# Kernel tuning notes

Hardware: AMD Instinct MI355X
Metric: run time of the kernel (lower is better)

The kernel has to match this reference:

```python
import jax, jax.numpy as jnp
import numpy as np

N, E = 50000, 250000
HID, H, C, IN, ED, L = 64, 4, 64, 6, 4, 2  # C = per-head out_channels


def _layer_norm(x, g, b, eps=1e-5):
    m = x.mean(-1, keepdims=True)
    v = x.var(-1, keepdims=True)
    return (x - m) / jnp.sqrt(v + eps) * g + b


def setup_inputs() -> dict:
    key = jax.random.key(0)
    ks = iter(jax.random.split(key, 32))
    rn = lambda shape, s=0.05: (jax.random.normal(next(ks), shape, dtype=jnp.float32) * s)
    inp = {
        "x": rn((N, IN), 1.0),
        "edge_index": jax.random.randint(next(ks), (2, E), 0, N, dtype=jnp.int64),
        "edge_attr": rn((E, ED), 1.0),
        "enc_w1": rn((IN, HID)), "enc_b1": jnp.zeros((HID,), jnp.float32),
        "enc_ln_g": jnp.ones((HID,), jnp.float32), "enc_ln_b": jnp.zeros((HID,), jnp.float32),
        "enc_w2": rn((HID, HID)), "enc_b2": jnp.zeros((HID,), jnp.float32),
        "Wq": rn((L, HID, H * C)), "bq": jnp.zeros((L, H * C), jnp.float32),
        "Wk": rn((L, HID, H * C)), "bk": jnp.zeros((L, H * C), jnp.float32),
        "Wv": rn((L, HID, H * C)), "bv": jnp.zeros((L, H * C), jnp.float32),
        "We": rn((L, ED, H * C)),
        "Wskip": rn((L, HID, HID)), "bskip": jnp.zeros((L, HID), jnp.float32),
        "Wbeta": rn((L, 3 * HID, 1)),
        "ln_g": jnp.ones((L, HID), jnp.float32), "ln_b": jnp.zeros((L, HID), jnp.float32),
        "head_w1": rn((HID, HID // 2)), "head_b1": jnp.zeros((HID // 2,), jnp.float32),
        "head_w2": rn((HID // 2, 2)), "head_b2": jnp.zeros((2,), jnp.float32),
    }
    return inp


def _transformer_conv(h, src, dst, ea, Wq, bq, Wk, bk, Wv, bv, We, Ws, bs, Wb):
    n = h.shape[0]
    q = (h @ Wq + bq).reshape(n, H, C)
    k = (h @ Wk + bk).reshape(n, H, C)
    v = (h @ Wv + bv).reshape(n, H, C)
    e = (ea @ We).reshape(-1, H, C)          # [E,H,C] edge projection (no bias)
    kj = k[src] + e                           # gather keys at source + edge
    alpha = (q[dst] * kj).sum(-1) / jnp.sqrt(jnp.float32(C))   # [E,H]
    # segment softmax over edges sharing a destination node
    m = jax.ops.segment_max(alpha, dst, num_segments=n)
    m = jnp.where(jnp.isfinite(m), m, 0.0)
    ex = jnp.exp(alpha - m[dst])
    s = jax.ops.segment_sum(ex, dst, num_segments=n)
    attn = ex / (s[dst] + 1e-16)              # [E,H]
    msg = (v[src] + e) * attn[:, :, None]
    out = jax.ops.segment_sum(msg, dst, num_segments=n).mean(axis=1)  # concat=False -> head mean
    xr = h @ Ws + bs                          # skip projection
    beta = jax.nn.sigmoid(jnp.concatenate([out, xr, out - xr], axis=-1) @ Wb)  # [N,1]
    return beta * xr + (1.0 - beta) * out


def reference(x, edge_index, edge_attr, enc_w1, enc_b1, enc_ln_g, enc_ln_b, enc_w2, enc_b2,
              Wq, bq, Wk, bk, Wv, bv, We, Wskip, bskip, Wbeta, ln_g, ln_b,
              head_w1, head_b1, head_w2, head_b2):
    src, dst = edge_index[0], edge_index[1]
    # node encoder (dropout = identity in eval)
    h = jax.nn.gelu(x @ enc_w1 + enc_b1, approximate=False)
    h = _layer_norm(h, enc_ln_g, enc_ln_b)
    h = h @ enc_w2 + enc_b2
    # stacked TransformerConv + residual + LayerNorm
    for l in range(Wq.shape[0]):
        h_new = _transformer_conv(h, src, dst, edge_attr,
                                  Wq[l], bq[l], Wk[l], bk[l], Wv[l], bv[l],
                                  We[l], Wskip[l], bskip[l], Wbeta[l])
        h = _layer_norm(h + h_new, ln_g[l], ln_b[l])
    # output head
    o = jax.nn.gelu(h @ head_w1 + head_b1, approximate=False)
    return o @ head_w2 + head_b2
```

## Files before the change

kernel.cpp:

```cpp
#include <hip/hip_runtime.h>
#include <hip/hip_bf16.h>
#include <math.h>

#define NN 50000
#define EE 250000
#define SBLK 256
#define NBLK ((NN + SBLK - 1) / SBLK)

typedef __attribute__((ext_vector_type(8))) short bf16x8;
typedef __attribute__((ext_vector_type(4))) float f32x4;

__device__ __forceinline__ float wsum64(float v) {
  v += __shfl_xor(v, 1, 64);
  v += __shfl_xor(v, 2, 64);
  v += __shfl_xor(v, 4, 64);
  v += __shfl_xor(v, 8, 64);
  v += __shfl_xor(v, 16, 64);
  v += __shfl_xor(v, 32, 64);
  return v;
}

__device__ __forceinline__ int wsum64i(int v) {
  v += __shfl_xor(v, 1, 64);
  v += __shfl_xor(v, 2, 64);
  v += __shfl_xor(v, 4, 64);
  v += __shfl_xor(v, 8, 64);
  v += __shfl_xor(v, 16, 64);
  v += __shfl_xor(v, 32, 64);
  return v;
}

__device__ __forceinline__ int wscan_inc(int v, int lane) {
  #pragma unroll
  for (int d = 1; d < 64; d <<= 1) {
    int u = __shfl_up(v, d, 64);
    if (lane >= d) v += u;
  }
  return v;
}

__device__ __forceinline__ float gelu_exact(float a) {
  return 0.5f * a * (1.0f + erff(a * 0.70710678118654752f));
}

__device__ __forceinline__ ushort f2bf(float f) {
  __hip_bfloat16 h = __float2bfloat16(f);
  return *reinterpret_cast<ushort*>(&h);
}

__device__ __forceinline__ void bf4_to_f(const uint2 u, float* f) {
  f[0] = __uint_as_float(u.x << 16);
  f[1] = __uint_as_float(u.x & 0xffff0000u);
  f[2] = __uint_as_float(u.y << 16);
  f[3] = __uint_as_float(u.y & 0xffff0000u);
}

__global__ __launch_bounds__(256) void convert_wb_kernel(
    const float* __restrict__ Wq, const float* __restrict__ Wk,
    const float* __restrict__ Wv, const float* __restrict__ Ws,
    __hip_bfloat16* __restrict__ Wb) {
  const int tid = blockIdx.x * 256 + threadIdx.x;
  const int layer = tid / 53248;
  const int rem = tid % 53248;
  const int i = rem & 7;
  const int l = (rem >> 3) & 63;
  const int fct = rem >> 9;
  const int f = fct & 1;
  const int ct = fct >> 1;
  const int col = ct * 16 + (l & 15);
  const int kk = f * 32 + (l >> 4) * 8 + i;
  float val;
  if (col < 256)      val = Wq[(size_t)layer * 16384 + kk * 256 + col];
  else if (col < 512) val = Wk[(size_t)layer * 16384 + kk * 256 + (col - 256)];
  else if (col < 768) val = Wv[(size_t)layer * 16384 + kk * 256 + (col - 512)];
  else                val = Ws[(size_t)layer * 4096 + kk * 64 + (col - 768)];
  Wb[tid] = __float2bfloat16(val);
}

__global__ __launch_bounds__(256) void hist_kernel(const int* __restrict__ ei,
                                                   int* __restrict__ cnt) {
  const int e = blockIdx.x * 256 + threadIdx.x;
  if (e < EE) atomicAdd(&cnt[ei[EE + e]], 1);
}

__global__ __launch_bounds__(256) void bsum_kernel(const int* __restrict__ cnt,
                                                   int* __restrict__ bsum) {
  const int i = blockIdx.x * 256 + threadIdx.x;
  int v = (i < NN) ? cnt[i] : 0;
  v = wsum64i(v);
  __shared__ int ws_[4];
  if ((threadIdx.x & 63) == 0) ws_[threadIdx.x >> 6] = v;
  __syncthreads();
  if (threadIdx.x == 0) bsum[blockIdx.x] = ws_[0] + ws_[1] + ws_[2] + ws_[3];
}

__global__ __launch_bounds__(256) void bscan_kernel(const int* __restrict__ bsum,
                                                    int* __restrict__ bpre) {
  const int t = threadIdx.x;
  const int lane = t & 63;
  const int w = t >> 6;
  int orig = (t < NBLK) ? bsum[t] : 0;
  int v = wscan_inc(orig, lane);
  __shared__ int wtot[4];
  if (lane == 63) wtot[w] = v;
  __syncthreads();
  int add = 0;
  #pragma unroll
  for (int j = 0; j < 4; j++) if (j < w) add += wtot[j];
  if (t < NBLK) bpre[t] = v + add - orig;
}

__global__ __launch_bounds__(256) void scan2_kernel(const int* __restrict__ cnt,
                                                    const int* __restrict__ bpre,
                                                    int* __restrict__ offs,
                                                    int* __restrict__ cursor) {
  const int i = blockIdx.x * 256 + threadIdx.x;
  const int t = threadIdx.x;
  const int lane = t & 63;
  const int w = t >> 6;
  int orig = (i < NN) ? cnt[i] : 0;
  int v = wscan_inc(orig, lane);
  __shared__ int wtot[4];
  if (lane == 63) wtot[w] = v;
  __syncthreads();
  int add = bpre[blockIdx.x];
  #pragma unroll
  for (int j = 0; j < 4; j++) if (j < w) add += wtot[j];
  int ex = v + add - orig;
  if (i < NN) { offs[i] = ex; cursor[i] = ex; }
  if (i == 0) offs[NN] = EE;
}

__global__ __launch_bounds__(256) void scatter_kernel(
    const int* __restrict__ ei, const float* __restrict__ ea,
    int* __restrict__ cursor, int* __restrict__ src_sorted,
    float4* __restrict__ ea_sorted) {
  const int e = blockIdx.x * 256 + threadIdx.x;
  if (e >= EE) return;
  const int dst = ei[EE + e];
  const int pos = atomicAdd(&cursor[dst], 1);
  src_sorted[pos] = ei[e];
  ea_sorted[pos] = reinterpret_cast<const float4*>(ea)[e];
}

__global__ __launch_bounds__(256) void enc_kernel(
    const float* __restrict__ x, const float* __restrict__ w1,
    const float* __restrict__ b1, const float* __restrict__ lg,
    const float* __restrict__ lb, const float* __restrict__ w2,
    const float* __restrict__ b2, float* __restrict__ h,
    __hip_bfloat16* __restrict__ hb) {
  const int t = blockIdx.x * 256 + threadIdx.x;
  const int node = t >> 6;
  const int lane = t & 63;
  const int wib = (threadIdx.x >> 6);
  __shared__ float gS[4][64];
  if (node < NN) {
    float a = b1[lane];
    #pragma unroll
    for (int d = 0; d < 6; d++) a += x[(size_t)node * 6 + d] * w1[d * 64 + lane];
    float g = gelu_exact(a);
    float s1 = wsum64(g);
    float s2 = wsum64(g * g);
    float m = s1 * (1.0f / 64.0f);
    float var = s2 * (1.0f / 64.0f) - m * m;
    g = (g - m) * rsqrtf(var + 1e-5f) * lg[lane] + lb[lane];
    gS[wib][lane] = g;
  }
  __syncthreads();
  if (node < NN) {
    float a = b2[lane];
    #pragma unroll 8
    for (int d = 0; d < 64; d++) a += gS[wib][d] * w2[d * 64 + lane];
    h[(size_t)node * 64 + lane] = a;
    hb[(size_t)node * 64 + lane] = __float2bfloat16(a);
  }
}

__global__ __launch_bounds__(256) void proj_mfma_kernel(
    const __hip_bfloat16* __restrict__ hbf,
    const __hip_bfloat16* __restrict__ Wb,
    const float* __restrict__ bq, const float* __restrict__ bk,
    const float* __restrict__ bv, const float* __restrict__ bs,
    __hip_bfloat16* __restrict__ q, __hip_bfloat16* __restrict__ k,
    __hip_bfloat16* __restrict__ v, float* __restrict__ xr) {
  const int n0 = blockIdx.x * 64;
  const int w = threadIdx.x >> 6;
  const int l = threadIdx.x & 63;
  const int r = l & 15;
  const int g = l >> 4;
  const int node = n0 + w * 16 + r;
  const int cg = g * 4;
  const bool in = (node < NN);

  bf16x8 A0 = {}, A1 = {};
  if (in) {
    const bf16x8* ap = reinterpret_cast<const bf16x8*>(hbf + (size_t)node * 64);
    A0 = ap[g];
    A1 = ap[g + 4];
  }

  const bf16x8* wb = reinterpret_cast<const bf16x8*>(Wb);

  for (int ct = 0; ct < 52; ++ct) {
    bf16x8 B0 = wb[(ct * 2 + 0) * 64 + l];
    bf16x8 B1 = wb[(ct * 2 + 1) * 64 + l];
    f32x4 acc = {0.f, 0.f, 0.f, 0.f};
    acc = __builtin_amdgcn_mfma_f32_16x16x32_bf16(B0, A0, acc, 0, 0, 0);
    acc = __builtin_amdgcn_mfma_f32_16x16x32_bf16(B1, A1, acc, 0, 0, 0);
    if (!in) continue;
    if (ct < 48) {
      __hip_bfloat16* dstp;
      const float* bias;
      int cb;
      float scale = 1.0f;
      if (ct < 16)      { dstp = q; bias = bq; cb = ct * 16 + cg; scale = 0.125f; }
      else if (ct < 32) { dstp = k; bias = bk; cb = (ct - 16) * 16 + cg; }
      else              { dstp = v; bias = bv; cb = (ct - 32) * 16 + cg; }
      const float4 bb = *reinterpret_cast<const float4*>(bias + cb);
      uint2 pk;
      pk.x = (uint)f2bf((acc[0] + bb.x) * scale) |
             ((uint)f2bf((acc[1] + bb.y) * scale) << 16);
      pk.y = (uint)f2bf((acc[2] + bb.z) * scale) |
             ((uint)f2bf((acc[3] + bb.w) * scale) << 16);
      *reinterpret_cast<uint2*>(dstp + (size_t)node * 256 + cb) = pk;
    } else {
      const int cb = (ct - 48) * 16 + cg;
      const float4 bb = *reinterpret_cast<const float4*>(bs + cb);
      float4 o = {acc[0] + bb.x, acc[1] + bb.y, acc[2] + bb.z, acc[3] + bb.w};
      *reinterpret_cast<float4*>(xr + (size_t)node * 64 + cb) = o;
    }
  }
}

__global__ __launch_bounds__(256) void edge_fused_kernel(
    const int* __restrict__ offs, const int* __restrict__ src_sorted,
    const float4* __restrict__ ea_sorted,
    const __hip_bfloat16* __restrict__ qb, const __hip_bfloat16* __restrict__ kb,
    const __hip_bfloat16* __restrict__ vb, const float* __restrict__ We,
    float* __restrict__ agg) {
  const int node = (blockIdx.x * 256 + threadIdx.x) >> 6;
  const int lane = threadIdx.x & 63;
  if (node >= NN) return;
  const int c0 = lane * 4;
  const ushort* q = reinterpret_cast<const ushort*>(qb);
  const ushort* k = reinterpret_cast<const ushort*>(kb);
  const ushort* v = reinterpret_cast<const ushort*>(vb);

  const float4 w0 = *reinterpret_cast<const float4*>(We + 0 * 256 + c0);
  const float4 w1 = *reinterpret_cast<const float4*>(We + 1 * 256 + c0);
  const float4 w2 = *reinterpret_cast<const float4*>(We + 2 * 256 + c0);
  const float4 w3 = *reinterpret_cast<const float4*>(We + 3 * 256 + c0);

  const int beg = offs[node];
  const int end = offs[node + 1];
  float qf[4];
  {
    uint2 qu = *reinterpret_cast<const uint2*>(q + (size_t)node * 256 + c0);
    bf4_to_f(qu, qf);
  }
  float m0 = 0.f, m1 = 0.f, m2 = 0.f, m3 = 0.f, sacc = 0.f;
  for (int e = beg; e < end; ++e) {
    const int src = src_sorted[e];
    const float4 av = ea_sorted[e];
    const float eh0 = av.x * w0.x + av.y * w1.x + av.z * w2.x + av.w * w3.x;
    const float eh1 = av.x * w0.y + av.y * w1.y + av.z * w2.y + av.w * w3.y;
    const float eh2 = av.x * w0.z + av.y * w1.z + av.z * w2.z + av.w * w3.z;
    const float eh3 = av.x * w0.w + av.y * w1.w + av.z * w2.w + av.w * w3.w;
    uint2 ku = *reinterpret_cast<const uint2*>(k + (size_t)src * 256 + c0);
    uint2 vu = *reinterpret_cast<const uint2*>(v + (size_t)src * 256 + c0);
    float kf[4], vf[4];
    bf4_to_f(ku, kf);
    bf4_to_f(vu, vf);
    float d = qf[0] * (kf[0] + eh0) + qf[1] * (kf[1] + eh1) +
              qf[2] * (kf[2] + eh2) + qf[3] * (kf[3] + eh3);
    d += __shfl_xor(d, 1, 64);
    d += __shfl_xor(d, 2, 64);
    d += __shfl_xor(d, 4, 64);
    d += __shfl_xor(d, 8, 64);
    const float ex = __expf(d);
    sacc += ex;
    m0 += ex * (vf[0] + eh0);
    m1 += ex * (vf[1] + eh1);
    m2 += ex * (vf[2] + eh2);
    m3 += ex * (vf[3] + eh3);
  }
  const float inv = 0.25f / (sacc + 1e-16f);
  m0 *= inv; m1 *= inv; m2 *= inv; m3 *= inv;
  m0 += __shfl_xor(m0, 16, 64); m0 += __shfl_xor(m0, 32, 64);
  m1 += __shfl_xor(m1, 16, 64); m1 += __shfl_xor(m1, 32, 64);
  m2 += __shfl_xor(m2, 16, 64); m2 += __shfl_xor(m2, 32, 64);
  m3 += __shfl_xor(m3, 16, 64); m3 += __shfl_xor(m3, 32, 64);
  if (lane < 16) {
    float4 o = {m0, m1, m2, m3};
    *reinterpret_cast<float4*>(agg + (size_t)node * 64 + lane * 4) = o;
  }
}

__global__ __launch_bounds__(256) void node_kernel(
    const float* __restrict__ agg, const float* __restrict__ xr,
    float* __restrict__ h, __hip_bfloat16* __restrict__ hb,
    const float* __restrict__ Wb,
    const float* __restrict__ lg, const float* __restrict__ lb) {
  const int t = blockIdx.x * 256 + threadIdx.x;
  const int node = t >> 6;
  const int lane = t & 63;
  if (node >= NN) return;
  float o = agg[(size_t)node * 64 + lane];
  float x = xr[(size_t)node * 64 + lane];
  float p = o * Wb[lane] + x * Wb[64 + lane] + (o - x) * Wb[128 + lane];
  p = wsum64(p);
  float beta = 1.0f / (1.0f + expf(-p));
  float hn = beta * x + (1.0f - beta) * o;
  float val = h[(size_t)node * 64 + lane] + hn;
  float s1 = wsum64(val);
  float s2 = wsum64(val * val);
  float m = s1 * (1.0f / 64.0f);
  float var = s2 * (1.0f / 64.0f) - m * m;
  float res = (val - m) * rsqrtf(var + 1e-5f) * lg[lane] + lb[lane];
  h[(size_t)node * 64 + lane] = res;
  hb[(size_t)node * 64 + lane] = __float2bfloat16(res);
}

__global__ __launch_bounds__(256) void head_kernel(
    const float* __restrict__ h, const float* __restrict__ w1,
    const float* __restrict__ b1, const float* __restrict__ w2,
    const float* __restrict__ b2, float* __restrict__ out) {
  const int base_node = blockIdx.x * 8;
  const int nib = threadIdx.x >> 5;
  const int c = threadIdx.x & 31;
  __shared__ float hS[8][64];
  #pragma unroll
  for (int i = 0; i < 2; i++) {
    int idx = threadIdx.x + i * 256;
    int nn = idx >> 6, d = idx & 63;
    if (base_node + nn < NN) hS[nn][d] = h[(size_t)(base_node + nn) * 64 + d];
  }
  __syncthreads();
  const int node = base_node + nib;
  if (node < NN) {
    float a = b1[c];
    #pragma unroll 8
    for (int d = 0; d < 64; d++) a += hS[nib][d] * w1[d * 32 + c];
    float g = gelu_exact(a);
    float p0 = g * w2[c * 2 + 0];
    float p1 = g * w2[c * 2 + 1];
    #pragma unroll
    for (int m = 1; m < 32; m <<= 1) {
      p0 += __shfl_xor(p0, m, 64);
      p1 += __shfl_xor(p1, m, 64);
    }
    if (c == 0) {
      out[(size_t)node * 2 + 0] = p0 + b2[0];
      out[(size_t)node * 2 + 1] = p1 + b2[1];
    }
  }
}

extern "C" void kernel_launch(void* const* d_in, const int* in_sizes, int n_in,
                              void* d_out, int out_size, void* d_ws, size_t ws_size,
                              hipStream_t stream) {
  const float* x       = (const float*)d_in[0];
  const int*   ei      = (const int*)d_in[1];
  const float* ea      = (const float*)d_in[2];
  const float* enc_w1  = (const float*)d_in[3];
  const float* enc_b1  = (const float*)d_in[4];
  const float* enc_lng = (const float*)d_in[5];
  const float* enc_lnb = (const float*)d_in[6];
  const float* enc_w2  = (const float*)d_in[7];
  const float* enc_b2  = (const float*)d_in[8];
  const float* Wq      = (const float*)d_in[9];
  const float* bq      = (const float*)d_in[10];
  const float* Wk      = (const float*)d_in[11];
  const float* bk      = (const float*)d_in[12];
  const float* Wv      = (const float*)d_in[13];
  const float* bv      = (const float*)d_in[14];
  const float* We      = (const float*)d_in[15];
  const float* Wskip   = (const float*)d_in[16];
  const float* bskip   = (const float*)d_in[17];
  const float* Wbeta   = (const float*)d_in[18];
  const float* ln_g    = (const float*)d_in[19];
  const float* ln_b    = (const float*)d_in[20];
  const float* hw1     = (const float*)d_in[21];
  const float* hb1     = (const float*)d_in[22];
  const float* hw2     = (const float*)d_in[23];
  const float* hb2     = (const float*)d_in[24];
  float* out = (float*)d_out;

  float* ws  = (float*)d_ws;
  float* h   = ws;
  float* xr  = h + (size_t)NN * 64;
  float* agg = xr + (size_t)NN * 64;
  float* fend = agg + (size_t)NN * 64;
  __hip_bfloat16* hb = (__hip_bfloat16*)fend;
  __hip_bfloat16* qb = hb + (size_t)NN * 64;
  __hip_bfloat16* kb = qb + (size_t)NN * 256;
  __hip_bfloat16* vb = kb + (size_t)NN * 256;
  __hip_bfloat16* Wb = vb + (size_t)NN * 256;
  int* cnt        = (int*)(Wb + 2 * 53248);
  int* offs       = cnt + NN;
  int* cursor     = offs + NN + 1;
  int* bsum       = cursor + NN;
  int* bpre       = bsum + NBLK;
  int* src_sorted = bpre + NBLK;
  float4* ea_sorted = (float4*)(src_sorted + EE + 3);

  hipMemsetAsync(cnt, 0, (size_t)NN * sizeof(int), stream);
  hist_kernel<<<977, 256, 0, stream>>>(ei, cnt);
  bsum_kernel<<<NBLK, 256, 0, stream>>>(cnt, bsum);
  bscan_kernel<<<1, 256, 0, stream>>>(bsum, bpre);
  scan2_kernel<<<NBLK, 256, 0, stream>>>(cnt, bpre, offs, cursor);
  scatter_kernel<<<977, 256, 0, stream>>>(ei, ea, cursor, src_sorted, ea_sorted);

  convert_wb_kernel<<<416, 256, 0, stream>>>(Wq, Wk, Wv, Wskip, Wb);
  enc_kernel<<<12500, 256, 0, stream>>>(x, enc_w1, enc_b1, enc_lng, enc_lnb,
                                        enc_w2, enc_b2, h, hb);

  for (int l = 0; l < 2; l++) {
    proj_mfma_kernel<<<782, 256, 0, stream>>>(
        hb, Wb + (size_t)l * 53248,
        bq + (size_t)l * 256, bk + (size_t)l * 256, bv + (size_t)l * 256,
        bskip + (size_t)l * 64, qb, kb, vb, xr);
    edge_fused_kernel<<<12500, 256, 0, stream>>>(
        offs, src_sorted, ea_sorted, qb, kb, vb, We + (size_t)l * 1024, agg);
    node_kernel<<<12500, 256, 0, stream>>>(agg, xr, h, hb, Wbeta + (size_t)l * 192,
                                           ln_g + (size_t)l * 64,
                                           ln_b + (size_t)l * 64);
  }

  head_kernel<<<6250, 256, 0, stream>>>(h, hw1, hb1, hw2, hb2, out);
}
```

Measured before the change: 414.0 us.

## Fuse node update into edge kernel, interleave K/V, split projection blocks

Merges the beta-gating plus residual LayerNorm node kernel into the edge aggregation kernel, so the agg buffer is never written or re-read and one launch per layer goes away. K and V are stored interleaved per node, so each edge gathers both with one 16-byte load instead of two 8-byte loads. The projection kernel is split across twice as many blocks, each doing half the column tiles, and it software-prefetches the next weight tile. The risks are more register pressure in the fused kernel and the A tile being loaded twice in the projection.

```diff
diff --git a/kernel.cpp b/kernel.cpp
--- a/kernel.cpp
+++ b/kernel.cpp
@@ -181,9 +181,11 @@
     const __hip_bfloat16* __restrict__ Wb,
     const float* __restrict__ bq, const float* __restrict__ bk,
     const float* __restrict__ bv, const float* __restrict__ bs,
-    __hip_bfloat16* __restrict__ q, __hip_bfloat16* __restrict__ k,
-    __hip_bfloat16* __restrict__ v, float* __restrict__ xr) {
-  const int n0 = blockIdx.x * 64;
+    __hip_bfloat16* __restrict__ q, __hip_bfloat16* __restrict__ kv,
+    float* __restrict__ xr) {
+  const int nb = blockIdx.x >> 1;
+  const int half = blockIdx.x & 1;
+  const int n0 = nb * 64;
   const int w = threadIdx.x >> 6;
   const int l = threadIdx.x & 63;
   const int r = l & 15;
@@ -200,29 +202,43 @@
   }
 
   const bf16x8* wb = reinterpret_cast<const bf16x8*>(Wb);
-
-  for (int ct = 0; ct < 52; ++ct) {
-    bf16x8 B0 = wb[(ct * 2 + 0) * 64 + l];
-    bf16x8 B1 = wb[(ct * 2 + 1) * 64 + l];
+  const int ct0 = half * 26, ct1 = ct0 + 26;
+
+  bf16x8 B0 = wb[(ct0 * 2 + 0) * 64 + l];
+  bf16x8 B1 = wb[(ct0 * 2 + 1) * 64 + l];
+  for (int ct = ct0; ct < ct1; ++ct) {
+    bf16x8 C0 = B0, C1 = B1;
+    if (ct + 1 < ct1) {
+      B0 = wb[((ct + 1) * 2 + 0) * 64 + l];
+      B1 = wb[((ct + 1) * 2 + 1) * 64 + l];
+    }
     f32x4 acc = {0.f, 0.f, 0.f, 0.f};
-    acc = __builtin_amdgcn_mfma_f32_16x16x32_bf16(B0, A0, acc, 0, 0, 0);
-    acc = __builtin_amdgcn_mfma_f32_16x16x32_bf16(B1, A1, acc, 0, 0, 0);
+    acc = __builtin_amdgcn_mfma_f32_16x16x32_bf16(C0, A0, acc, 0, 0, 0);
+    acc = __builtin_amdgcn_mfma_f32_16x16x32_bf16(C1, A1, acc, 0, 0, 0);
     if (!in) continue;
-    if (ct < 48) {
-      __hip_bfloat16* dstp;
-      const float* bias;
-      int cb;
-      float scale = 1.0f;
-      if (ct < 16)      { dstp = q; bias = bq; cb = ct * 16 + cg; scale = 0.125f; }
-      else if (ct < 32) { dstp = k; bias = bk; cb = (ct - 16) * 16 + cg; }
-      else              { dstp = v; bias = bv; cb = (ct - 32) * 16 + cg; }
-      const float4 bb = *reinterpret_cast<const float4*>(bias + cb);
+    if (ct < 16) {
+      const int cb = ct * 16 + cg;
+      const float4 bb = *reinterpret_cast<const float4*>(bq + cb);
       uint2 pk;
-      pk.x = (uint)f2bf((acc[0] + bb.x) * scale) |
-             ((uint)f2bf((acc[1] + bb.y) * scale) << 16);
-      pk.y = (uint)f2bf((acc[2] + bb.z) * scale) |
-             ((uint)f2bf((acc[3] + bb.w) * scale) << 16);
-      *reinterpret_cast<uint2*>(dstp + (size_t)node * 256 + cb) = pk;
+      pk.x = (uint)f2bf((acc[0] + bb.x) * 0.125f) |
+             ((uint)f2bf((acc[1] + bb.y) * 0.125f) << 16);
+      pk.y = (uint)f2bf((acc[2] + bb.z) * 0.125f) |
+             ((uint)f2bf((acc[3] + bb.w) * 0.125f) << 16);
+      *reinterpret_cast<uint2*>(q + (size_t)node * 256 + cb) = pk;
+    } else if (ct < 32) {
+      const int cb = (ct - 16) * 16 + cg;
+      const float4 bb = *reinterpret_cast<const float4*>(bk + cb);
+      uint2 pk;
+      pk.x = (uint)f2bf(acc[0] + bb.x) | ((uint)f2bf(acc[1] + bb.y) << 16);
+      pk.y = (uint)f2bf(acc[2] + bb.z) | ((uint)f2bf(acc[3] + bb.w) << 16);
+      *reinterpret_cast<uint2*>(kv + (size_t)node * 512 + cb * 2) = pk;
+    } else if (ct < 48) {
+      const int cb = (ct - 32) * 16 + cg;
+      const float4 bb = *reinterpret_cast<const float4*>(bv + cb);
+      uint2 pk;
+      pk.x = (uint)f2bf(acc[0] + bb.x) | ((uint)f2bf(acc[1] + bb.y) << 16);
+      pk.y = (uint)f2bf(acc[2] + bb.z) | ((uint)f2bf(acc[3] + bb.w) << 16);
+      *reinterpret_cast<uint2*>(kv + (size_t)node * 512 + cb * 2 + 4) = pk;
     } else {
       const int cb = (ct - 48) * 16 + cg;
       const float4 bb = *reinterpret_cast<const float4*>(bs + cb);
@@ -232,19 +248,19 @@
   }
 }
 
-__global__ __launch_bounds__(256) void edge_fused_kernel(
+__global__ __launch_bounds__(256) void edge_node_kernel(
     const int* __restrict__ offs, const int* __restrict__ src_sorted,
     const float4* __restrict__ ea_sorted,
-    const __hip_bfloat16* __restrict__ qb, const __hip_bfloat16* __restrict__ kb,
-    const __hip_bfloat16* __restrict__ vb, const float* __restrict__ We,
-    float* __restrict__ agg) {
+    const __hip_bfloat16* __restrict__ qb, const __hip_bfloat16* __restrict__ kvb,
+    const float* __restrict__ We, const float* __restrict__ xr,
+    float* __restrict__ h, __hip_bfloat16* __restrict__ hb,
+    const float* __restrict__ Wbt, const float* __restrict__ lg,
+    const float* __restrict__ lb) {
   const int node = (blockIdx.x * 256 + threadIdx.x) >> 6;
   const int lane = threadIdx.x & 63;
   if (node >= NN) return;
   const int c0 = lane * 4;
   const ushort* q = reinterpret_cast<const ushort*>(qb);
-  const ushort* k = reinterpret_cast<const ushort*>(kb);
-  const ushort* v = reinterpret_cast<const ushort*>(vb);
 
   const float4 w0 = *reinterpret_cast<const float4*>(We + 0 * 256 + c0);
   const float4 w1 = *reinterpret_cast<const float4*>(We + 1 * 256 + c0);
@@ -266,11 +282,11 @@
     const float eh1 = av.x * w0.y + av.y * w1.y + av.z * w2.y + av.w * w3.y;
     const float eh2 = av.x * w0.z + av.y * w1.z + av.z * w2.z + av.w * w3.z;
     const float eh3 = av.x * w0.w + av.y * w1.w + av.z * w2.w + av.w * w3.w;
-    uint2 ku = *reinterpret_cast<const uint2*>(k + (size_t)src * 256 + c0);
-    uint2 vu = *reinterpret_cast<const uint2*>(v + (size_t)src * 256 + c0);
+    const uint4 kv = *reinterpret_cast<const uint4*>(
+        kvb + (size_t)src * 512 + c0 * 2);
     float kf[4], vf[4];
-    bf4_to_f(ku, kf);
-    bf4_to_f(vu, vf);
+    bf4_to_f(make_uint2(kv.x, kv.y), kf);
+    bf4_to_f(make_uint2(kv.z, kv.w), vf);
     float d = qf[0] * (kf[0] + eh0) + qf[1] * (kf[1] + eh1) +
               qf[2] * (kf[2] + eh2) + qf[3] * (kf[3] + eh3);
     d += __shfl_xor(d, 1, 64);
@@ -290,35 +306,46 @@
   m1 += __shfl_xor(m1, 16, 64); m1 += __shfl_xor(m1, 32, 64);
   m2 += __shfl_xor(m2, 16, 64); m2 += __shfl_xor(m2, 32, 64);
   m3 += __shfl_xor(m3, 16, 64); m3 += __shfl_xor(m3, 32, 64);
+
+  const int cb = (lane & 15) * 4;
+  const float4 x4 = *reinterpret_cast<const float4*>(xr + (size_t)node * 64 + cb);
+  const float4 h4 = *reinterpret_cast<const float4*>(h + (size_t)node * 64 + cb);
+  float p = m0 * Wbt[cb + 0] + x4.x * Wbt[64 + cb + 0] + (m0 - x4.x) * Wbt[128 + cb + 0]
+          + m1 * Wbt[cb + 1] + x4.y * Wbt[64 + cb + 1] + (m1 - x4.y) * Wbt[128 + cb + 1]
+          + m2 * Wbt[cb + 2] + x4.z * Wbt[64 + cb + 2] + (m2 - x4.z) * Wbt[128 + cb + 2]
+          + m3 * Wbt[cb + 3] + x4.w * Wbt[64 + cb + 3] + (m3 - x4.w) * Wbt[128 + cb + 3];
+  p += __shfl_xor(p, 1, 64);
+  p += __shfl_xor(p, 2, 64);
+  p += __shfl_xor(p, 4, 64);
+  p += __shfl_xor(p, 8, 64);
+  const float beta = 1.0f / (1.0f + __expf(-p));
+  float v0 = h4.x + beta * x4.x + (1.0f - beta) * m0;
+  float v1 = h4.y + beta * x4.y + (1.0f - beta) * m1;
+  float v2 = h4.z + beta * x4.z + (1.0f - beta) * m2;
+  float v3 = h4.w + beta * x4.w + (1.0f - beta) * m3;
+  float s1 = v0 + v1 + v2 + v3;
+  float s2 = v0 * v0 + v1 * v1 + v2 * v2 + v3 * v3;
+  s1 += __shfl_xor(s1, 1, 64); s2 += __shfl_xor(s2, 1, 64);
+  s1 += __shfl_xor(s1, 2, 64); s2 += __shfl_xor(s2, 2, 64);
+  s1 += __shfl_xor(s1, 4, 64); s2 += __shfl_xor(s2, 4, 64);
+  s1 += __shfl_xor(s1, 8, 64); s2 += __shfl_xor(s2, 8, 64);
+  const float mean = s1 * (1.0f / 64.0f);
+  const float var = s2 * (1.0f / 64.0f) - mean * mean;
+  const float rstd = rsqrtf(var + 1e-5f);
+  const float4 g4 = *reinterpret_cast<const float4*>(lg + cb);
+  const float4 b4 = *reinterpret_cast<const float4*>(lb + cb);
+  const float r0 = (v0 - mean) * rstd * g4.x + b4.x;
+  const float r1 = (v1 - mean) * rstd * g4.y + b4.y;
+  const float r2 = (v2 - mean) * rstd * g4.z + b4.z;
+  const float r3 = (v3 - mean) * rstd * g4.w + b4.w;
   if (lane < 16) {
-    float4 o = {m0, m1, m2, m3};
-    *reinterpret_cast<float4*>(agg + (size_t)node * 64 + lane * 4) = o;
-  }
-}
-
-__global__ __launch_bounds__(256) void node_kernel(
-    const float* __restrict__ agg, const float* __restrict__ xr,
-    float* __restrict__ h, __hip_bfloat16* __restrict__ hb,
-    const float* __restrict__ Wb,
-    const float* __restrict__ lg, const float* __restrict__ lb) {
-  const int t = blockIdx.x * 256 + threadIdx.x;
-  const int node = t >> 6;
-  const int lane = t & 63;
-  if (node >= NN) return;
-  float o = agg[(size_t)node * 64 + lane];
-  float x = xr[(size_t)node * 64 + lane];
-  float p = o * Wb[lane] + x * Wb[64 + lane] + (o - x) * Wb[128 + lane];
-  p = wsum64(p);
-  float beta = 1.0f / (1.0f + expf(-p));
-  float hn = beta * x + (1.0f - beta) * o;
-  float val = h[(size_t)node * 64 + lane] + hn;
-  float s1 = wsum64(val);
-  float s2 = wsum64(val * val);
-  float m = s1 * (1.0f / 64.0f);
-  float var = s2 * (1.0f / 64.0f) - m * m;
-  float res = (val - m) * rsqrtf(var + 1e-5f) * lg[lane] + lb[lane];
-  h[(size_t)node * 64 + lane] = res;
-  hb[(size_t)node * 64 + lane] = __float2bfloat16(res);
+    float4 o = {r0, r1, r2, r3};
+    *reinterpret_cast<float4*>(h + (size_t)node * 64 + cb) = o;
+    uint2 pk;
+    pk.x = (uint)f2bf(r0) | ((uint)f2bf(r1) << 16);
+    pk.y = (uint)f2bf(r2) | ((uint)f2bf(r3) << 16);
+    *reinterpret_cast<uint2*>(hb + (size_t)node * 64 + cb) = pk;
+  }
 }
 
 __global__ __launch_bounds__(256) void head_kernel(
@@ -389,13 +416,11 @@
   float* ws  = (float*)d_ws;
   float* h   = ws;
   float* xr  = h + (size_t)NN * 64;
-  float* agg = xr + (size_t)NN * 64;
-  float* fend = agg + (size_t)NN * 64;
+  float* fend = xr + (size_t)NN * 64;
   __hip_bfloat16* hb = (__hip_bfloat16*)fend;
   __hip_bfloat16* qb = hb + (size_t)NN * 64;
-  __hip_bfloat16* kb = qb + (size_t)NN * 256;
-  __hip_bfloat16* vb = kb + (size_t)NN * 256;
-  __hip_bfloat16* Wb = vb + (size_t)NN * 256;
+  __hip_bfloat16* kvb = qb + (size_t)NN * 256;
+  __hip_bfloat16* Wb = kvb + (size_t)NN * 512;
   int* cnt        = (int*)(Wb + 2 * 53248);
   int* offs       = cnt + NN;
   int* cursor     = offs + NN + 1;
@@ -416,15 +441,14 @@
                                         enc_w2, enc_b2, h, hb);
 
   for (int l = 0; l < 2; l++) {
-    proj_mfma_kernel<<<782, 256, 0, stream>>>(
+    proj_mfma_kernel<<<1564, 256, 0, stream>>>(
         hb, Wb + (size_t)l * 53248,
         bq + (size_t)l * 256, bk + (size_t)l * 256, bv + (size_t)l * 256,
-        bskip + (size_t)l * 64, qb, kb, vb, xr);
-    edge_fused_kernel<<<12500, 256, 0, stream>>>(
-        offs, src_sorted, ea_sorted, qb, kb, vb, We + (size_t)l * 1024, agg);
-    node_kernel<<<12500, 256, 0, stream>>>(agg, xr, h, hb, Wbeta + (size_t)l * 192,
-                                           ln_g + (size_t)l * 64,
-                                           ln_b + (size_t)l * 64);
+        bskip + (size_t)l * 64, qb, kvb, xr);
+    edge_node_kernel<<<12500, 256, 0, stream>>>(
+        offs, src_sorted, ea_sorted, qb, kvb, We + (size_t)l * 1024, xr,
+        h, hb, Wbeta + (size_t)l * 192, ln_g + (size_t)l * 64,
+        ln_b + (size_t)l * 64);
   }
 
   head_kernel<<<6250, 256, 0, stream>>>(h, hw1, hb1, hw2, hb2, out);
```

Result: faster. 389.9 us (-5.8%).
